# Kernel tuning notes

Hardware: AMD Instinct MI355X
Metric: run time of the kernel (lower is better)

## Reference

```python
import jax, jax.numpy as jnp
import numpy as np

B, T, D_IN, D_HID, D_OUT = 16, 4096, 512, 512, 512


def _gru(x, w_ih, w_hh, b_ih, b_hh):
    """Single-layer unidirectional GRU, batch_first, h0=0. PyTorch gate order (r,z,n).
    x: [B,T,Din]; w_ih: [3H,Din]; w_hh: [3H,H]; b_ih,b_hh: [3H]. Returns [B,T,H]."""
    Bs = x.shape[0]
    H = w_hh.shape[1]
    # Precompute input projections for all timesteps (one big GEMM).
    xp = jnp.einsum('btd,gd->btg', x, w_ih) + b_ih  # [B,T,3H]

    def step(h, xt):
        gh = h @ w_hh.T + b_hh                      # [B,3H]
        xr, xz, xn = jnp.split(xt, 3, axis=-1)
        hr, hz, hn = jnp.split(gh, 3, axis=-1)
        r = jax.nn.sigmoid(xr + hr)
        z = jax.nn.sigmoid(xz + hz)
        n = jnp.tanh(xn + r * hn)
        h_new = (1.0 - z) * n + z * h
        return h_new, h_new

    h0 = jnp.zeros((Bs, H), x.dtype)
    _, ys = jax.lax.scan(step, h0, jnp.swapaxes(xp, 0, 1))  # [T,B,H]
    return jnp.swapaxes(ys, 0, 1)


def setup_inputs() -> dict:
    key = jax.random.key(0)
    ks = jax.random.split(key, 9)
    s1 = 1.0 / np.sqrt(D_HID)
    s2 = 1.0 / np.sqrt(D_OUT)
    return {
        'x': jax.random.normal(ks[0], (B, T, D_IN), dtype=jnp.float32),
        'w_ih1': jax.random.uniform(ks[1], (3 * D_HID, D_IN), jnp.float32, -s1, s1),
        'w_hh1': jax.random.uniform(ks[2], (3 * D_HID, D_HID), jnp.float32, -s1, s1),
        'b_ih1': jax.random.uniform(ks[3], (3 * D_HID,), jnp.float32, -s1, s1),
        'b_hh1': jax.random.uniform(ks[4], (3 * D_HID,), jnp.float32, -s1, s1),
        'w_ih2': jax.random.uniform(ks[5], (3 * D_OUT, D_HID), jnp.float32, -s2, s2),
        'w_hh2': jax.random.uniform(ks[6], (3 * D_OUT, D_OUT), jnp.float32, -s2, s2),
        'b_ih2': jax.random.uniform(ks[7], (3 * D_OUT,), jnp.float32, -s2, s2),
        'b_hh2': jax.random.uniform(ks[8], (3 * D_OUT,), jnp.float32, -s2, s2),
    }


def reference(x, w_ih1, w_hh1, b_ih1, b_hh1, w_ih2, w_hh2, b_ih2, b_hh2):
    h = _gru(x, w_ih1, w_hh1, b_ih1, b_hh1)
    h = jax.nn.gelu(h, approximate=False)  # nn.GELU default = exact erf
    # drop1/drop2 are identity (drop=0.0, eval); norm is Identity (norm_layer=None)
    y = _gru(h, w_ih2, w_hh2, b_ih2, b_hh2)
    return y
```

## Files before the change

kernel.cpp:

```cpp
#include <hip/hip_runtime.h>
#include <math.h>

#define BATCH 16
#define TLEN 4096
#define KDIM 512
#define G3 1536

#define UBK 16
#define GRP 8
#define NBLK (UBK * GRP)
#define UPB 32
#define BPB 2
#define ROWS 96
#define REC_THREADS 768

#define HP 516
#define PP 37

#define H_OFF 0
#define PART_OFF (BPB * HP)
#define GH_OFF (PART_OFF + 192 * PP)
#define XQ_OFF (GH_OFF + 192)
#define BH_OFF (XQ_OFF + 192)
#define SMEM_FLOATS (BH_OFF + ROWS)
#define SMEM_BYTES (SMEM_FLOATS * 4)

typedef __attribute__((ext_vector_type(4))) float f32x4;
typedef __attribute__((ext_vector_type(2))) unsigned u32x2;
typedef __attribute__((ext_vector_type(4))) unsigned u32x4;

__device__ __forceinline__ float fast_sigmoid(float x) {
  float e = __expf(-x);
  return __builtin_amdgcn_rcpf(1.f + e);
}
__device__ __forceinline__ float fast_tanh(float x) {
  float ax = fabsf(x);
  float e = __expf(-2.f * ax);
  float r = (1.f - e) * __builtin_amdgcn_rcpf(1.f + e);
  return copysignf(r, x);
}

__global__ __launch_bounds__(256)
void gemm_nt_bias(const float* __restrict__ A, const float* __restrict__ W,
                  const float* __restrict__ bias, float* __restrict__ C,
                  int M, int N) {
  const int K = KDIM;
  __shared__ float As[16][132];
  __shared__ float Bs[16][132];
  int tid = threadIdx.x;
  int tx = tid & 15, ty = tid >> 4;
  int bx = blockIdx.x, by = blockIdx.y;
  const float* Ab = A + (size_t)by * 128 * K;
  const float* Wb = W + (size_t)bx * 128 * K;

  float acc[8][8];
#pragma unroll
  for (int i = 0; i < 8; i++)
#pragma unroll
    for (int j = 0; j < 8; j++) acc[i][j] = 0.f;

  for (int kk = 0; kk < K; kk += 16) {
    __syncthreads();
#pragma unroll
    for (int i = 0; i < 2; i++) {
      int task = tid + i * 256;
      int kc = task & 3;
      int mrow = task >> 2;
      float4 va = *(const float4*)(Ab + (size_t)mrow * K + kk + kc * 4);
      As[kc*4+0][mrow] = va.x; As[kc*4+1][mrow] = va.y;
      As[kc*4+2][mrow] = va.z; As[kc*4+3][mrow] = va.w;
      float4 vb = *(const float4*)(Wb + (size_t)mrow * K + kk + kc * 4);
      Bs[kc*4+0][mrow] = vb.x; Bs[kc*4+1][mrow] = vb.y;
      Bs[kc*4+2][mrow] = vb.z; Bs[kc*4+3][mrow] = vb.w;
    }
    __syncthreads();
#pragma unroll
    for (int k = 0; k < 16; k++) {
      float4 a0 = *(const float4*)&As[k][ty * 4];
      float4 a1 = *(const float4*)&As[k][64 + ty * 4];
      float4 b0 = *(const float4*)&Bs[k][tx * 4];
      float4 b1 = *(const float4*)&Bs[k][64 + tx * 4];
      float av[8] = {a0.x, a0.y, a0.z, a0.w, a1.x, a1.y, a1.z, a1.w};
      float bv[8] = {b0.x, b0.y, b0.z, b0.w, b1.x, b1.y, b1.z, b1.w};
#pragma unroll
      for (int i = 0; i < 8; i++)
#pragma unroll
        for (int j = 0; j < 8; j++) acc[i][j] += av[i] * bv[j];
    }
  }

#pragma unroll
  for (int hi = 0; hi < 2; hi++)
#pragma unroll
    for (int i = 0; i < 4; i++) {
      int mrow = by * 128 + hi * 64 + ty * 4 + i;
      int b = mrow >> 12;
      int t = mrow & (TLEN - 1);
#pragma unroll
      for (int hj = 0; hj < 2; hj++) {
        int n = bx * 128 + hj * 64 + tx * 4;
        int g = n >> 9;
        int unit = n & 511;
        float4 bb = *(const float4*)(bias + n);
        float4 v;
        v.x = acc[hi*4+i][hj*4+0] + bb.x;
        v.y = acc[hi*4+i][hj*4+1] + bb.y;
        v.z = acc[hi*4+i][hj*4+2] + bb.z;
        v.w = acc[hi*4+i][hj*4+3] + bb.w;
        size_t dst = (((((size_t)t * UBK + (unit >> 5)) * GRP + (b >> 1)) * 3 + g) * BPB
                      + (b & 1)) * UPB + (unit & 31);
        *(float4*)(C + dst) = v;
      }
    }
}

__global__ __launch_bounds__(REC_THREADS, 1)
void gru_rec(const float* __restrict__ xp,
             const float* __restrict__ w_hh,
             const float* __restrict__ b_hh,
             unsigned* __restrict__ mb,
             unsigned flag_base,
             float* __restrict__ out,
             int apply_gelu) {
  extern __shared__ float sm[];
  float* h_s   = sm + H_OFF;
  float* part_s= sm + PART_OFF;
  float* gh_s  = sm + GH_OFF;
  float* xq_s  = sm + XQ_OFF;
  float* bhh_s = sm + BH_OFF;

  const int tid = threadIdx.x;
  const int L = blockIdx.x;
  const int g = L & 7;
  const int m = L >> 3;
  const int u0 = m * UPB;
  const int b0 = g * BPB;
  const float* xslice = xp + ((size_t)m * GRP + g) * (3 * BPB * UPB);

  const int tile = tid >> 5;
  const int ks = tid & 31;

  float4 wreg[4][4];
#pragma unroll
  for (int r = 0; r < 4; r++) {
    int row = tile * 4 + r;
    int gate = row >> 5, u = row & 31;
    const float* wrow = w_hh + (size_t)(gate * KDIM + u0 + u) * KDIM;
#pragma unroll
    for (int kk = 0; kk < 4; kk++)
      wreg[r][kk] = *(const float4*)(wrow + (size_t)(kk * 32 + ks) * 4);
  }
  if (tid < ROWS) bhh_s[tid] = b_hh[(tid >> 5) * KDIM + u0 + (tid & 31)];

  float4 xq_reg = {0.f, 0.f, 0.f, 0.f};
  if (tid < 48) xq_reg = *(const float4*)(xslice + tid * 4);

  float hprev = 0.f;

  for (int t = 0; t < TLEN; t++) {
    if (t == 0) {
      for (int idx = tid; idx < BPB * KDIM; idx += REC_THREADS)
        h_s[(idx >> 9) * HP + (idx & 511)] = 0.f;
    } else {
      if (tid < 512) {
        const unsigned* src = mb + ((size_t)(((t + 1) & 1) * GRP + g) * 1024
                                    + (size_t)tid * 2) * 2;
        const unsigned tgt = flag_base + (unsigned)t;
        u32x4 pv;
        for (;;) {
          asm volatile("global_load_dwordx4 %0, %1, off sc0 sc1\n\ts_waitcnt vmcnt(0)"
                       : "=v"(pv) : "v"(src) : "memory");
          if (pv.y >= tgt && pv.w >= tgt) break;
          __builtin_amdgcn_s_sleep(1);
        }
        int j0 = tid * 2;
        int mm = j0 >> 6, bb = (j0 >> 5) & 1, uu = j0 & 31;
        float2 hv;
        hv.x = __uint_as_float(pv.x);
        hv.y = __uint_as_float(pv.z);
        *(float2*)(h_s + bb * HP + mm * 32 + uu) = hv;
      }
    }
    if (tid < 48) *(float4*)(xq_s + tid * 4) = xq_reg;
    __syncthreads();

    if (tid < 48 && t + 1 < TLEN)
      xq_reg = *(const float4*)(xslice + (size_t)(t + 1) * (UBK * GRP * 3 * BPB * UPB) + tid * 4);

    float4 a00={0,0,0,0},a01={0,0,0,0};
    float4 a10={0,0,0,0},a11={0,0,0,0};
    float4 a20={0,0,0,0},a21={0,0,0,0};
    float4 a30={0,0,0,0},a31={0,0,0,0};
#pragma unroll
    for (int kk = 0; kk < 4; kk++) {
      int k4 = kk * 32 + ks;
      float4 h0v = *(const float4*)(h_s + 0 * HP + k4 * 4);
      float4 h1v = *(const float4*)(h_s + 1 * HP + k4 * 4);
#define FMA4(d, wv, hv) d.x += wv.x*hv.x; d.y += wv.y*hv.y; d.z += wv.z*hv.z; d.w += wv.w*hv.w;
      FMA4(a00, wreg[0][kk], h0v) FMA4(a01, wreg[0][kk], h1v)
      FMA4(a10, wreg[1][kk], h0v) FMA4(a11, wreg[1][kk], h1v)
      FMA4(a20, wreg[2][kk], h0v) FMA4(a21, wreg[2][kk], h1v)
      FMA4(a30, wreg[3][kk], h0v) FMA4(a31, wreg[3][kk], h1v)
#undef FMA4
    }
    {
      float* pb = part_s + (size_t)(tile * 8) * PP + ks;
#define HS(v) ((v.x + v.y) + (v.z + v.w))
      pb[(0*2+0)*PP] = HS(a00); pb[(0*2+1)*PP] = HS(a01);
      pb[(1*2+0)*PP] = HS(a10); pb[(1*2+1)*PP] = HS(a11);
      pb[(2*2+0)*PP] = HS(a20); pb[(2*2+1)*PP] = HS(a21);
      pb[(3*2+0)*PP] = HS(a30); pb[(3*2+1)*PP] = HS(a31);
#undef HS
    }
    __syncthreads();

    if (tid < 192) {
      const float* p = part_s + (size_t)tid * PP;
      float s = 0.f;
#pragma unroll
      for (int j = 0; j < 32; j++) s += p[j];
      gh_s[tid] = s + bhh_s[tid >> 1];
    }
    __syncthreads();

    if (tid < 64) {
      int u = tid & 31, b = tid >> 5;
      float xr = xq_s[0 * 64 + b * 32 + u];
      float xz = xq_s[1 * 64 + b * 32 + u];
      float xn = xq_s[2 * 64 + b * 32 + u];
      float ghr = gh_s[(0 * 32 + u) * 2 + b];
      float ghz = gh_s[(1 * 32 + u) * 2 + b];
      float ghn = gh_s[(2 * 32 + u) * 2 + b];
      float rg = fast_sigmoid(xr + ghr);
      float zg = fast_sigmoid(xz + ghz);
      float ng = fast_tanh(xn + rg * ghn);
      float hn = (1.f - zg) * ng + zg * hprev;
      u32x2 pvs;
      pvs.x = __float_as_uint(hn);
      pvs.y = flag_base + (unsigned)t + 1u;
      unsigned* dst = mb + ((size_t)((t & 1) * GRP + g) * 1024
                            + (size_t)(m * 64 + b * 32 + u)) * 2;
      asm volatile("global_store_dwordx2 %0, %1, off sc0 sc1"
                   :: "v"(dst), "v"(pvs) : "memory");
      hprev = hn;
      float ov = hn;
      if (apply_gelu) ov = 0.5f * hn * (1.f + erff(hn * 0.70710678118654752f));
      out[((size_t)((b0 + b) * TLEN + t)) * KDIM + u0 + u] = ov;
    }
  }
}

extern "C" void kernel_launch(void* const* d_in, const int* in_sizes, int n_in,
                              void* d_out, int out_size, void* d_ws, size_t ws_size,
                              hipStream_t stream) {
  const float* x     = (const float*)d_in[0];
  const float* w_ih1 = (const float*)d_in[1];
  const float* w_hh1 = (const float*)d_in[2];
  const float* b_ih1 = (const float*)d_in[3];
  const float* b_hh1 = (const float*)d_in[4];
  const float* w_ih2 = (const float*)d_in[5];
  const float* w_hh2 = (const float*)d_in[6];
  const float* b_ih2 = (const float*)d_in[7];
  const float* b_hh2 = (const float*)d_in[8];
  float* y = (float*)d_out;

  char* ws = (char*)d_ws;
  const size_t XPB = (size_t)BATCH * TLEN * G3 * sizeof(float);
  float*    xp = (float*)ws;
  unsigned* mb = (unsigned*)(ws + XPB);

  hipFuncSetAttribute((const void*)gru_rec,
                      hipFuncAttributeMaxDynamicSharedMemorySize, SMEM_BYTES);
  hipMemsetAsync(mb, 0, (size_t)2 * GRP * UBK * 64 * 2 * sizeof(unsigned), stream);

  dim3 gg(12, 512), tb(256);
  const int M = BATCH * TLEN;

  gemm_nt_bias<<<gg, tb, 0, stream>>>(x, w_ih1, b_ih1, xp, M, G3);
  gru_rec<<<dim3(NBLK), REC_THREADS, SMEM_BYTES, stream>>>(xp, w_hh1, b_hh1, mb, 0u, y, 1);
  gemm_nt_bias<<<gg, tb, 0, stream>>>(y, w_ih2, b_ih2, xp, M, G3);
  gru_rec<<<dim3(NBLK), REC_THREADS, SMEM_BYTES, stream>>>(xp, w_hh2, b_hh2, mb, (unsigned)TLEN, y, 0);
}
```

Before: 19.12 ms.

## Spread GRU recurrence over 256 blocks with shuffle reductions and folded r/z biases

Doubles the number of recurrent blocks (16 units per block instead of 32), halving per-thread weight registers and per-block work on the serial critical path. The shared-memory partial-sum pass and one barrier are replaced by wavefront xor-shuffle reductions. The r and z hidden biases are folded into the input-projection GEMM, leaving only the n-gate bias in the loop. The spin-wait sleep is removed and dynamic shared memory is padded to a large fixed size, likely to force one block per CU. This adds more cross-block flag traffic per step and requires 256 co-resident blocks.

After: 20.91 ms. 1.09x slower.

```diff
diff --git a/kernel.cpp b/kernel.cpp
--- a/kernel.cpp
+++ b/kernel.cpp
@@ -6,24 +6,22 @@
 #define KDIM 512
 #define G3 1536
 
-#define UBK 16
+#define UBK 32
 #define GRP 8
 #define NBLK (UBK * GRP)
-#define UPB 32
+#define UPB 16
 #define BPB 2
-#define ROWS 96
+#define ROWS 48
 #define REC_THREADS 768
 
 #define HP 516
-#define PP 37
 
 #define H_OFF 0
-#define PART_OFF (BPB * HP)
-#define GH_OFF (PART_OFF + 192 * PP)
-#define XQ_OFF (GH_OFF + 192)
-#define BH_OFF (XQ_OFF + 192)
-#define SMEM_FLOATS (BH_OFF + ROWS)
-#define SMEM_BYTES (SMEM_FLOATS * 4)
+#define GH_OFF (BPB * HP)
+#define XQ_OFF (GH_OFF + 96)
+#define BHN_OFF (XQ_OFF + 96)
+#define SMEM_FLOATS (BHN_OFF + 16)
+#define SMEM_BYTES 86016
 
 typedef __attribute__((ext_vector_type(4))) float f32x4;
 typedef __attribute__((ext_vector_type(2))) unsigned u32x2;
@@ -42,8 +40,8 @@
 
 __global__ __launch_bounds__(256)
 void gemm_nt_bias(const float* __restrict__ A, const float* __restrict__ W,
-                  const float* __restrict__ bias, float* __restrict__ C,
-                  int M, int N) {
+                  const float* __restrict__ bias, const float* __restrict__ bias_hh,
+                  float* __restrict__ C, int M, int N) {
   const int K = KDIM;
   __shared__ float As[16][132];
   __shared__ float Bs[16][132];
@@ -102,13 +100,15 @@
         int g = n >> 9;
         int unit = n & 511;
         float4 bb = *(const float4*)(bias + n);
+        float4 b2 = {0.f, 0.f, 0.f, 0.f};
+        if (n < 1024) b2 = *(const float4*)(bias_hh + n);
         float4 v;
-        v.x = acc[hi*4+i][hj*4+0] + bb.x;
-        v.y = acc[hi*4+i][hj*4+1] + bb.y;
-        v.z = acc[hi*4+i][hj*4+2] + bb.z;
-        v.w = acc[hi*4+i][hj*4+3] + bb.w;
-        size_t dst = (((((size_t)t * UBK + (unit >> 5)) * GRP + (b >> 1)) * 3 + g) * BPB
-                      + (b & 1)) * UPB + (unit & 31);
+        v.x = acc[hi*4+i][hj*4+0] + bb.x + b2.x;
+        v.y = acc[hi*4+i][hj*4+1] + bb.y + b2.y;
+        v.z = acc[hi*4+i][hj*4+2] + bb.z + b2.z;
+        v.w = acc[hi*4+i][hj*4+3] + bb.w + b2.w;
+        size_t dst = ((((size_t)t * UBK + (unit >> 4)) * GRP + (b >> 1)) * 3 + g)
+                     * (BPB * UPB) + (size_t)(b & 1) * UPB + (unit & 15);
         *(float4*)(C + dst) = v;
       }
     }
@@ -124,36 +124,35 @@
              int apply_gelu) {
   extern __shared__ float sm[];
   float* h_s   = sm + H_OFF;
-  float* part_s= sm + PART_OFF;
   float* gh_s  = sm + GH_OFF;
   float* xq_s  = sm + XQ_OFF;
-  float* bhh_s = sm + BH_OFF;
+  float* bhn_s = sm + BHN_OFF;
 
   const int tid = threadIdx.x;
   const int L = blockIdx.x;
   const int g = L & 7;
-  const int m = L >> 3;
-  const int u0 = m * UPB;
+  const int memb = L >> 3;
+  const int u0 = memb * UPB;
   const int b0 = g * BPB;
-  const float* xslice = xp + ((size_t)m * GRP + g) * (3 * BPB * UPB);
+  const float* xslice = xp + ((size_t)memb * GRP + g) * (3 * BPB * UPB);
 
   const int tile = tid >> 5;
   const int ks = tid & 31;
 
-  float4 wreg[4][4];
-#pragma unroll
-  for (int r = 0; r < 4; r++) {
-    int row = tile * 4 + r;
-    int gate = row >> 5, u = row & 31;
+  float4 wreg[2][4];
+#pragma unroll
+  for (int r = 0; r < 2; r++) {
+    int row = tile * 2 + r;
+    int gate = row >> 4, u = row & 15;
     const float* wrow = w_hh + (size_t)(gate * KDIM + u0 + u) * KDIM;
 #pragma unroll
     for (int kk = 0; kk < 4; kk++)
       wreg[r][kk] = *(const float4*)(wrow + (size_t)(kk * 32 + ks) * 4);
   }
-  if (tid < ROWS) bhh_s[tid] = b_hh[(tid >> 5) * KDIM + u0 + (tid & 31)];
+  if (tid < UPB) bhn_s[tid] = b_hh[2 * KDIM + u0 + tid];
 
   float4 xq_reg = {0.f, 0.f, 0.f, 0.f};
-  if (tid < 48) xq_reg = *(const float4*)(xslice + tid * 4);
+  if (tid < 24) xq_reg = *(const float4*)(xslice + tid * 4);
 
   float hprev = 0.f;
 
@@ -171,75 +170,70 @@
           asm volatile("global_load_dwordx4 %0, %1, off sc0 sc1\n\ts_waitcnt vmcnt(0)"
                        : "=v"(pv) : "v"(src) : "memory");
           if (pv.y >= tgt && pv.w >= tgt) break;
-          __builtin_amdgcn_s_sleep(1);
         }
         int j0 = tid * 2;
-        int mm = j0 >> 6, bb = (j0 >> 5) & 1, uu = j0 & 31;
+        int mm = j0 >> 5, bb = (j0 >> 4) & 1, uu = j0 & 15;
         float2 hv;
         hv.x = __uint_as_float(pv.x);
         hv.y = __uint_as_float(pv.z);
-        *(float2*)(h_s + bb * HP + mm * 32 + uu) = hv;
+        *(float2*)(h_s + bb * HP + mm * 16 + uu) = hv;
       }
     }
-    if (tid < 48) *(float4*)(xq_s + tid * 4) = xq_reg;
-    __syncthreads();
-
-    if (tid < 48 && t + 1 < TLEN)
-      xq_reg = *(const float4*)(xslice + (size_t)(t + 1) * (UBK * GRP * 3 * BPB * UPB) + tid * 4);
-
-    float4 a00={0,0,0,0},a01={0,0,0,0};
-    float4 a10={0,0,0,0},a11={0,0,0,0};
-    float4 a20={0,0,0,0},a21={0,0,0,0};
-    float4 a30={0,0,0,0},a31={0,0,0,0};
+    if (tid < 24) *(float4*)(xq_s + tid * 4) = xq_reg;
+    __syncthreads();
+
+    if (tid < 24 && t + 1 < TLEN)
+      xq_reg = *(const float4*)(xslice + (size_t)(t + 1) * (NBLK * 3 * BPB * UPB) + tid * 4);
+
+    f32x4 hv0[4], hv1[4];
 #pragma unroll
     for (int kk = 0; kk < 4; kk++) {
       int k4 = kk * 32 + ks;
-      float4 h0v = *(const float4*)(h_s + 0 * HP + k4 * 4);
-      float4 h1v = *(const float4*)(h_s + 1 * HP + k4 * 4);
+      hv0[kk] = *(const f32x4*)(h_s + 0 * HP + k4 * 4);
+      hv1[kk] = *(const f32x4*)(h_s + 1 * HP + k4 * 4);
+    }
+    float4 a00={0,0,0,0}, a01={0,0,0,0}, a10={0,0,0,0}, a11={0,0,0,0};
+#pragma unroll
+    for (int kk = 0; kk < 4; kk++) {
 #define FMA4(d, wv, hv) d.x += wv.x*hv.x; d.y += wv.y*hv.y; d.z += wv.z*hv.z; d.w += wv.w*hv.w;
-      FMA4(a00, wreg[0][kk], h0v) FMA4(a01, wreg[0][kk], h1v)
-      FMA4(a10, wreg[1][kk], h0v) FMA4(a11, wreg[1][kk], h1v)
-      FMA4(a20, wreg[2][kk], h0v) FMA4(a21, wreg[2][kk], h1v)
-      FMA4(a30, wreg[3][kk], h0v) FMA4(a31, wreg[3][kk], h1v)
+      FMA4(a00, wreg[0][kk], hv0[kk]) FMA4(a01, wreg[0][kk], hv1[kk])
+      FMA4(a10, wreg[1][kk], hv0[kk]) FMA4(a11, wreg[1][kk], hv1[kk])
 #undef FMA4
     }
-    {
-      float* pb = part_s + (size_t)(tile * 8) * PP + ks;
-#define HS(v) ((v.x + v.y) + (v.z + v.w))
-      pb[(0*2+0)*PP] = HS(a00); pb[(0*2+1)*PP] = HS(a01);
-      pb[(1*2+0)*PP] = HS(a10); pb[(1*2+1)*PP] = HS(a11);
-      pb[(2*2+0)*PP] = HS(a20); pb[(2*2+1)*PP] = HS(a21);
-      pb[(3*2+0)*PP] = HS(a30); pb[(3*2+1)*PP] = HS(a31);
-#undef HS
-    }
-    __syncthreads();
-
-    if (tid < 192) {
-      const float* p = part_s + (size_t)tid * PP;
-      float s = 0.f;
-#pragma unroll
-      for (int j = 0; j < 32; j++) s += p[j];
-      gh_s[tid] = s + bhh_s[tid >> 1];
-    }
-    __syncthreads();
-
-    if (tid < 64) {
-      int u = tid & 31, b = tid >> 5;
-      float xr = xq_s[0 * 64 + b * 32 + u];
-      float xz = xq_s[1 * 64 + b * 32 + u];
-      float xn = xq_s[2 * 64 + b * 32 + u];
-      float ghr = gh_s[(0 * 32 + u) * 2 + b];
-      float ghz = gh_s[(1 * 32 + u) * 2 + b];
-      float ghn = gh_s[(2 * 32 + u) * 2 + b];
+    float s0 = (a00.x + a00.y) + (a00.z + a00.w);
+    float s1 = (a01.x + a01.y) + (a01.z + a01.w);
+    float s2 = (a10.x + a10.y) + (a10.z + a10.w);
+    float s3 = (a11.x + a11.y) + (a11.z + a11.w);
+#pragma unroll
+    for (int mk = 1; mk <= 16; mk <<= 1) {
+      s0 += __shfl_xor(s0, mk, 64);
+      s1 += __shfl_xor(s1, mk, 64);
+      s2 += __shfl_xor(s2, mk, 64);
+      s3 += __shfl_xor(s3, mk, 64);
+    }
+    if (ks < 4) {
+      float v = (ks == 0) ? s0 : (ks == 1) ? s1 : (ks == 2) ? s2 : s3;
+      gh_s[tile * 4 + ks] = v;
+    }
+    __syncthreads();
+
+    if (tid < 32) {
+      int u = tid & 15, b = tid >> 4;
+      float xr = xq_s[0 * 32 + b * 16 + u];
+      float xz = xq_s[1 * 32 + b * 16 + u];
+      float xn = xq_s[2 * 32 + b * 16 + u];
+      float ghr = gh_s[(0 * 16 + u) * 2 + b];
+      float ghz = gh_s[(1 * 16 + u) * 2 + b];
+      float ghn = gh_s[(2 * 16 + u) * 2 + b];
       float rg = fast_sigmoid(xr + ghr);
       float zg = fast_sigmoid(xz + ghz);
-      float ng = fast_tanh(xn + rg * ghn);
+      float ng = fast_tanh(xn + rg * (ghn + bhn_s[u]));
       float hn = (1.f - zg) * ng + zg * hprev;
       u32x2 pvs;
       pvs.x = __float_as_uint(hn);
       pvs.y = flag_base + (unsigned)t + 1u;
       unsigned* dst = mb + ((size_t)((t & 1) * GRP + g) * 1024
-                            + (size_t)(m * 64 + b * 32 + u)) * 2;
+                            + (size_t)(memb * 32 + b * 16 + u)) * 2;
       asm volatile("global_store_dwordx2 %0, %1, off sc0 sc1"
                    :: "v"(dst), "v"(pvs) : "memory");
       hprev = hn;
@@ -271,13 +265,13 @@
 
   hipFuncSetAttribute((const void*)gru_rec,
                       hipFuncAttributeMaxDynamicSharedMemorySize, SMEM_BYTES);
-  hipMemsetAsync(mb, 0, (size_t)2 * GRP * UBK * 64 * 2 * sizeof(unsigned), stream);
+  hipMemsetAsync(mb, 0, (size_t)2 * GRP * 1024 * 2 * sizeof(unsigned), stream);
 
   dim3 gg(12, 512), tb(256);
   const int M = BATCH * TLEN;
 
-  gemm_nt_bias<<<gg, tb, 0, stream>>>(x, w_ih1, b_ih1, xp, M, G3);
+  gemm_nt_bias<<<gg, tb, 0, stream>>>(x, w_ih1, b_ih1, b_hh1, xp, M, G3);
   gru_rec<<<dim3(NBLK), REC_THREADS, SMEM_BYTES, stream>>>(xp, w_hh1, b_hh1, mb, 0u, y, 1);
-  gemm_nt_bias<<<gg, tb, 0, stream>>>(y, w_ih2, b_ih2, xp, M, G3);
+  gemm_nt_bias<<<gg, tb, 0, stream>>>(y, w_ih2, b_ih2, b_hh2, xp, M, G3);
   gru_rec<<<dim3(NBLK), REC_THREADS, SMEM_BYTES, stream>>>(xp, w_hh2, b_hh2, mb, (unsigned)TLEN, y, 0);
 }
```
